# Optimization experiments

Hardware: AMD Instinct MI355X
Metric: run time of the kernel (lower is better)

## Reference

```python
import jax, jax.numpy as jnp
import numpy as np

DIM = 128; MOTION = 128; HEADS = 8; WS = 8; B2 = 4; H = 192; W = 192; HID = 512

def _ln(x, w, b, eps=1e-5):
    m = x.mean(-1, keepdims=True)
    v = ((x - m) ** 2).mean(-1, keepdims=True)
    return (x - m) / jnp.sqrt(v + eps) * w + b

def _win_part(x, ws):
    B, Hh, Ww, C = x.shape
    x = x.reshape(B, Hh // ws, ws, Ww // ws, ws, C).transpose(0, 1, 3, 2, 4, 5)
    return x.reshape(-1, ws * ws, C)

def _win_rev(win, ws, Hh, Ww):
    nwB, N, C = win.shape
    B = nwB // ((Hh // ws) * (Ww // ws))
    x = win.reshape(B, Hh // ws, Ww // ws, ws, ws, C).transpose(0, 1, 3, 2, 4, 5)
    return x.reshape(B, Hh, Ww, C)

def setup_inputs() -> dict:
    key = jax.random.key(0)
    ks = jax.random.split(key, 12)
    def lin(k, o, i):
        return jax.random.normal(k, (o, i), jnp.float32) * 0.02
    return {
        "x": jax.random.normal(ks[0], (B2, H * W, DIM), jnp.float32),
        "cor": jax.random.uniform(ks[1], (B2, H * W, 2), dtype=jnp.float32),
        "q_w": lin(ks[2], DIM, DIM),
        "kv_w": lin(ks[3], 2 * DIM, DIM),
        "cor_w": lin(ks[4], MOTION, 2),
        "proj_w": lin(ks[5], DIM, DIM), "proj_b": jnp.zeros((DIM,), jnp.float32),
        "mproj_w": lin(ks[6], MOTION, MOTION), "mproj_b": jnp.zeros((MOTION,), jnp.float32),
        "norm1_w": jnp.ones((DIM,), jnp.float32), "norm1_b": jnp.zeros((DIM,), jnp.float32),
        "norm2_w": jnp.ones((DIM,), jnp.float32), "norm2_b": jnp.zeros((DIM,), jnp.float32),
        "fc1_w": lin(ks[7], HID, DIM), "fc1_b": jnp.zeros((HID,), jnp.float32),
        "dw_w": jax.random.normal(ks[8], (HID, 1, 3, 3), jnp.float32) * 0.1,
        "dw_b": jnp.zeros((HID,), jnp.float32),
        "fc2_w": lin(ks[9], DIM, HID), "fc2_b": jnp.zeros((DIM,), jnp.float32),
    }

def _attn(x1, x2, cor, q_w, kv_w, cor_w, proj_w, proj_b, mproj_w, mproj_b):
    # x1,x2: (nwB, N, C) windowed query / cross-frame key-value; cor: (nwB, N, 2)
    B, N, C = x1.shape
    hd = C // HEADS
    mh = MOTION // HEADS
    scale = hd ** -0.5
    q = (x1 @ q_w.T).reshape(B, N, HEADS, hd).transpose(0, 2, 1, 3)
    kv = (x2 @ kv_w.T).reshape(B, N, 2, HEADS, hd).transpose(2, 0, 3, 1, 4)
    k, v = kv[0], kv[1]
    ce = cor @ cor_w.T                                   # (B, N, MOTION)
    ceh = ce.reshape(B, N, HEADS, mh).transpose(0, 2, 1, 3)
    attn = jax.nn.softmax(jnp.einsum('bhnd,bhmd->bhnm', q, k) * scale, axis=-1)
    xo = jnp.einsum('bhnm,bhmd->bhnd', attn, v).transpose(0, 2, 1, 3).reshape(B, N, C)
    crev = jnp.einsum('bhnm,bhmd->bhnd', attn, ceh).transpose(0, 2, 1, 3).reshape(B, N, MOTION)
    motion = (crev - ce) @ mproj_w.T + mproj_b
    return xo @ proj_w.T + proj_b, motion

def _mlp(x, fc1_w, fc1_b, dw_w, dw_b, fc2_w, fc2_b):
    B, N, _ = x.shape
    h = x @ fc1_w.T + fc1_b                              # (B, N, HID)
    hm = h.transpose(0, 2, 1).reshape(B, HID, H, W)
    hm = jax.lax.conv_general_dilated(hm, dw_w, (1, 1), 'SAME',
                                      feature_group_count=HID,
                                      dimension_numbers=('NCHW', 'OIHW', 'NCHW'))
    hm = hm + dw_b[None, :, None, None]
    h = jax.nn.gelu(hm.reshape(B, HID, N).transpose(0, 2, 1), approximate=False)
    return h @ fc2_w.T + fc2_b

def reference(x, cor, q_w, kv_w, cor_w, proj_w, proj_b, mproj_w, mproj_b,
              norm1_w, norm1_b, norm2_w, norm2_b, fc1_w, fc1_b, dw_w, dw_b, fc2_w, fc2_b):
    shortcut = x
    xn = _ln(x, norm1_w, norm1_b).reshape(B2, H, W, DIM)
    cm = cor.reshape(B2, H, W, 2)
    xw = _win_part(xn, WS)                               # (nwB, 64, DIM)
    cw = _win_part(cm, WS)
    nwB = xw.shape[0]
    xr = jnp.concatenate([xw[nwB // 2:], xw[:nwB // 2]], axis=0)
    xa, xm = _attn(xw, xr, cw, q_w, kv_w, cor_w, proj_w, proj_b, mproj_w, mproj_b)
    xa = _win_rev(xa, WS, H, W).reshape(B2, H * W, DIM)
    xm = _win_rev(xm, WS, H, W).reshape(B2, H * W, MOTION)
    x = shortcut + xa
    x = x + _mlp(_ln(x, norm2_w, norm2_b), fc1_w, fc1_b, dw_w, dw_b, fc2_w, fc2_b)
    return x, xm
```

## Files before the change

### kernel.cpp

```cpp
#include <hip/hip_runtime.h>
#include <hip/hip_bf16.h>
#include <math.h>

#define NB 4
#define IMG 192
#define HW (IMG*IMG)
#define T_TOT (NB*HW)
#define HID 512
#define NWB 2304
#define WPB 576
#define NWS 24

typedef __bf16 bf16;
typedef __bf16 bf8 __attribute__((ext_vector_type(8)));
typedef __bf16 bf4 __attribute__((ext_vector_type(4)));
typedef float f32x4 __attribute__((ext_vector_type(4)));

#define MFMA(a,b,c) __builtin_amdgcn_mfma_f32_16x16x32_bf16(a,b,c,0,0,0)

__device__ __forceinline__ int swz128(int row, int col){ return row*128 + (col ^ ((row&7)<<3)); }

__device__ __forceinline__ bf8 zero_bf8(){
  bf8 z = { (bf16)0.f,(bf16)0.f,(bf16)0.f,(bf16)0.f,(bf16)0.f,(bf16)0.f,(bf16)0.f,(bf16)0.f };
  return z;
}
__device__ __forceinline__ f32x4 zero_f4(){ f32x4 z = {0.f,0.f,0.f,0.f}; return z; }

__global__ void k_cvt(const float* __restrict__ s, bf16* __restrict__ d, int n, float scale){
  int i = blockIdx.x*256 + threadIdx.x;
  if (i < n) d[i] = (bf16)(s[i]*scale);
}

__global__ void k_a2(const float* __restrict__ mproj_w, const float* __restrict__ cor_w,
                     bf16* __restrict__ a2w){
  int idx = blockIdx.x*256 + threadIdx.x;
  if (idx >= 4096) return;
  int o = idx >> 5, k = idx & 31;
  float acc = 0.f;
  if (k < 16){
    int h = k >> 1, c = k & 1;
    #pragma unroll
    for (int i=0;i<16;i++)
      acc += mproj_w[o*128 + h*16 + i] * cor_w[(h*16+i)*2 + c];
  }
  a2w[o*32 + k] = (bf16)acc;
}

__global__ __launch_bounds__(256) void k_ln1(
    const float* __restrict__ x, const float* __restrict__ cor,
    const float* __restrict__ n1w, const float* __restrict__ n1b,
    bf16* __restrict__ xn, bf16* __restrict__ cwb)
{
  int tid = threadIdx.x, wm = tid>>6, l = tid&63;
  int lr = l & 15, tg = l >> 4;
  int t = blockIdx.x*16 + wm*4 + tg;

  const float* xp = x + (size_t)t*128 + lr*8;
  float4 a = *(const float4*)xp;
  float4 b4 = *(const float4*)(xp+4);
  float s  = a.x+a.y+a.z+a.w + b4.x+b4.y+b4.z+b4.w;
  float sq = a.x*a.x+a.y*a.y+a.z*a.z+a.w*a.w + b4.x*b4.x+b4.y*b4.y+b4.z*b4.z+b4.w*b4.w;
  #pragma unroll
  for (int m=1;m<16;m<<=1){ s += __shfl_xor(s,m,16); sq += __shfl_xor(sq,m,16); }
  float mean = s * (1.0f/128.0f);
  float var  = sq * (1.0f/128.0f) - mean*mean;
  float rstd = rsqrtf(var + 1e-5f);

  float4 nw0 = *(const float4*)(n1w + lr*8), nw1 = *(const float4*)(n1w + lr*8 + 4);
  float4 nb0 = *(const float4*)(n1b + lr*8), nb1 = *(const float4*)(n1b + lr*8 + 4);

  bf8 o;
  o[0] = (bf16)((a.x -mean)*rstd*nw0.x + nb0.x);
  o[1] = (bf16)((a.y -mean)*rstd*nw0.y + nb0.y);
  o[2] = (bf16)((a.z -mean)*rstd*nw0.z + nb0.z);
  o[3] = (bf16)((a.w -mean)*rstd*nw0.w + nb0.w);
  o[4] = (bf16)((b4.x-mean)*rstd*nw1.x + nb1.x);
  o[5] = (bf16)((b4.y-mean)*rstd*nw1.y + nb1.y);
  o[6] = (bf16)((b4.z-mean)*rstd*nw1.z + nb1.z);
  o[7] = (bf16)((b4.w-mean)*rstd*nw1.w + nb1.w);

  int b = t / HW, r = t % HW;
  int yy = r / IMG, xx = r % IMG;
  int win = b*WPB + (yy>>3)*NWS + (xx>>3);
  int n = ((yy&7)<<3) + (xx&7);
  *(bf8*)(xn + (size_t)win*8192 + n*128 + lr*8) = o;

  if (lr < 2) cwb[(size_t)win*128 + n*2 + lr] = (bf16)cor[(size_t)t*2 + lr];
}

__global__ __launch_bounds__(256) void k_attn(
    const bf16* __restrict__ xn, const bf16* __restrict__ cw,
    const bf16* __restrict__ wq, const bf16* __restrict__ wkv,
    const bf16* __restrict__ wpj, const bf16* __restrict__ a2w,
    const float* __restrict__ proj_b, const float* __restrict__ mproj_b,
    const float* __restrict__ x_in, float* __restrict__ x1, float* __restrict__ out_m)
{
  __shared__ __align__(16) bf16 s_s [64*128];
  __shared__ __align__(16) bf16 s_k [64*128];
  __shared__ __align__(16) bf16 s_vT[128*64];
  __shared__ __align__(16) bf16 s_P [2][64*64];
  __shared__ __align__(16) bf16 s_cT[16*64];
  __shared__ __align__(16) bf16 s_D [64*32];

  int tid = threadIdx.x, wm = tid>>6, l = tid&63;
  int lr = l & 15, lg = l >> 4;
  int win = blockIdx.x;
  int partner = (win + NWB/2) % NWB;
  const bf16* xw_g = xn + (size_t)win*8192;
  const bf16* xr_g = xn + (size_t)partner*8192;

  bf8 xrv[4], xwv[4];
  #pragma unroll
  for (int tci=0;tci<4;tci++){
    int chunk = tid + tci*256;
    int row = chunk>>4, c0 = (chunk&15)*8;
    xrv[tci] = *(const bf8*)(xr_g + row*128 + c0);
    xwv[tci] = *(const bf8*)(xw_g + row*128 + c0);
  }
  bf16 cwv = (bf16)0.f;
  if (tid < 128) cwv = cw[(size_t)win*128 + tid];

  *(unsigned long long*)&s_cT[tid*4] = 0ull;
  *(unsigned long long*)&s_D[tid*8]   = 0ull;
  *(unsigned long long*)&s_D[tid*8+4] = 0ull;
  #pragma unroll
  for (int tci=0;tci<4;tci++){
    int chunk = tid + tci*256;
    int row = chunk>>4, c0 = (chunk&15)*8;
    *(bf8*)&s_s[swz128(row,c0)] = xrv[tci];
  }
  __syncthreads();

  if (tid < 128){
    int c = tid & 1, m = tid >> 1;
    s_cT[c*64 + (m ^ (c<<3))] = cwv;
  } else if (tid < 192){
    int m = tid - 128;
    s_cT[2*64 + (m ^ 16)] = (bf16)1.0f;
  }
  {
    bf8 af[4];
    #pragma unroll
    for (int ks=0;ks<4;ks++) af[ks] = *(const bf8*)&s_s[swz128(wm*16+lr, ks*32 + lg*8)];
    #pragma unroll
    for (int nt=0;nt<8;nt++){
      f32x4 acc = zero_f4();
      #pragma unroll
      for (int ks=0;ks<4;ks++){
        bf8 bfr = *(const bf8*)(wkv + (nt*16+lr)*128 + ks*32 + lg*8);
        acc = MFMA(af[ks], bfr, acc);
      }
      #pragma unroll
      for (int j=0;j<4;j++){
        int row = wm*16 + lg*4 + j;
        s_k[swz128(row, nt*16+lr)] = (bf16)acc[j];
      }
    }
    #pragma unroll
    for (int nt=0;nt<8;nt++){
      f32x4 acc = zero_f4();
      #pragma unroll
      for (int ks=0;ks<4;ks++){
        bf8 bfr = *(const bf8*)(wkv + (128 + nt*16+lr)*128 + ks*32 + lg*8);
        acc = MFMA(af[ks], bfr, acc);
      }
      #pragma unroll
      for (int j=0;j<4;j++){
        int tok = wm*16 + lg*4 + j;
        int chc = nt*16 + lr;
        s_vT[chc*64 + (tok ^ ((chc&7)<<3))] = (bf16)acc[j];
      }
    }
  }
  __syncthreads();

  #pragma unroll
  for (int tci=0;tci<4;tci++){
    int chunk = tid + tci*256;
    int row = chunk>>4, c0 = (chunk&15)*8;
    *(bf8*)&s_s[swz128(row,c0)] = xwv[tci];
  }
  __syncthreads();

  {
    bf8 af[4];
    #pragma unroll
    for (int ks=0;ks<4;ks++) af[ks] = *(const bf8*)&s_s[swz128(wm*16+lr, ks*32 + lg*8)];
    #pragma unroll
    for (int nt=0;nt<8;nt++){
      f32x4 acc = zero_f4();
      #pragma unroll
      for (int ks=0;ks<4;ks++){
        bf8 bfr = *(const bf8*)(wq + (nt*16+lr)*128 + ks*32 + lg*8);
        acc = MFMA(af[ks], bfr, acc);
      }
      #pragma unroll
      for (int j=0;j<4;j++){
        int row = wm*16 + lg*4 + j;
        s_s[swz128(row, nt*16+lr)] = (bf16)acc[j];
      }
    }
  }

  float mycw[4] = {0.f,0.f,0.f,0.f};
  if (lr < 2){
    #pragma unroll
    for (int j=0;j<4;j++){
      int row = wm*16 + lg*4 + j;
      mycw[j] = (float)s_cT[lr*64 + (row ^ (lr<<3))];
    }
  }

  #pragma unroll
  for (int h=0;h<8;h++){
    bf8 aS = zero_bf8();
    if (l < 32) aS = *(const bf8*)&s_s[swz128(wm*16+lr, h*16 + lg*8)];
    f32x4 accS[4];
    #pragma unroll
    for (int nt=0;nt<4;nt++){
      bf8 bSv = zero_bf8();
      if (l < 32) bSv = *(const bf8*)&s_k[swz128(nt*16+lr, h*16 + lg*8)];
      accS[nt] = MFMA(aS, bSv, zero_f4());
    }
    bf16* Pb = &s_P[h&1][0];
    #pragma unroll
    for (int nt=0;nt<4;nt++){
      #pragma unroll
      for (int j=0;j<4;j++){
        int row = wm*16 + lg*4 + j;
        Pb[row*64 + ((nt*16+lr) ^ ((row&7)<<3))] = (bf16)__expf(accS[nt][j]);
      }
    }
    f32x4 accO = zero_f4(), accPC = zero_f4();
    #pragma unroll
    for (int ks=0;ks<2;ks++){
      int rowA = wm*16 + lr;
      bf8 aP = *(const bf8*)&Pb[rowA*64 + ((ks*32 + lg*8) ^ ((rowA&7)<<3))];
      int chc = h*16 + lr;
      bf8 bV = *(const bf8*)&s_vT[chc*64 + ((ks*32 + lg*8) ^ ((chc&7)<<3))];
      accO = MFMA(aP, bV, accO);
      bf8 bC = *(const bf8*)&s_cT[lr*64 + ((ks*32 + lg*8) ^ ((lr&7)<<3))];
      accPC = MFMA(aP, bC, accPC);
    }
    #pragma unroll
    for (int j=0;j<4;j++){
      int row = wm*16 + lg*4 + j;
      float rs = __shfl(accPC[j], (l & 48) + 2, 64);
      float inv = __builtin_amdgcn_rcpf(rs);
      s_s[swz128(row, h*16+lr)] = (bf16)(accO[j]*inv);
      if (lr < 2)
        s_D[row*32 + ((2*h+lr) ^ ((row&3)<<3))] = (bf16)(accPC[j]*inv - mycw[j]);
    }
  }

  int b  = win / WPB, wi = win % WPB;
  int wy = wi / NWS,  wx = wi % NWS;
  {
    bf8 af[4];
    #pragma unroll
    for (int ks=0;ks<4;ks++) af[ks] = *(const bf8*)&s_s[swz128(wm*16+lr, ks*32 + lg*8)];
    #pragma unroll
    for (int nt=0;nt<8;nt++){
      f32x4 acc = zero_f4();
      #pragma unroll
      for (int ks=0;ks<4;ks++){
        bf8 bfr = *(const bf8*)(wpj + (nt*16+lr)*128 + ks*32 + lg*8);
        acc = MFMA(af[ks], bfr, acc);
      }
      int col = nt*16 + lr;
      float pb = proj_b[col];
      #pragma unroll
      for (int j=0;j<4;j++){
        int tok = wm*16 + lg*4 + j;
        int yy = wy*8 + (tok>>3), xx = wx*8 + (tok&7);
        size_t addr = ((size_t)b*HW + yy*IMG + xx)*128 + col;
        x1[addr] = acc[j] + pb + x_in[addr];
      }
    }
  }
  {
    int rowA = wm*16 + lr;
    bf8 afD = *(const bf8*)&s_D[rowA*32 + ((lg*8) ^ ((rowA&3)<<3))];
    #pragma unroll
    for (int nt=0;nt<8;nt++){
      bf8 bfr = *(const bf8*)(a2w + (nt*16+lr)*32 + lg*8);
      f32x4 acc = MFMA(afD, bfr, zero_f4());
      int col = nt*16 + lr;
      float pb = mproj_b[col];
      #pragma unroll
      for (int j=0;j<4;j++){
        int tok = wm*16 + lg*4 + j;
        int yy = wy*8 + (tok>>3), xx = wx*8 + (tok&7);
        size_t addr = ((size_t)b*HW + yy*IMG + xx)*128 + col;
        out_m[addr] = acc[j] + pb;
      }
    }
  }
}

__global__ __launch_bounds__(256) void k_fc1(
    const float* __restrict__ x1, const float* __restrict__ n2w, const float* __restrict__ n2b,
    const bf16* __restrict__ wf1, const float* __restrict__ fc1b, bf16* __restrict__ h)
{
  __shared__ __align__(16) bf16 s_a[64*128];
  int tid = threadIdx.x, wm = tid>>6, l = tid&63;
  int lr = l & 15, lg = l >> 4;
  size_t t0 = (size_t)blockIdx.x * 64;

  float4 nw0 = *(const float4*)(n2w + lr*8), nw1 = *(const float4*)(n2w + lr*8 + 4);
  float4 nb0 = *(const float4*)(n2b + lr*8), nb1 = *(const float4*)(n2b + lr*8 + 4);

  #pragma unroll
  for (int rr=0; rr<4; rr++){
    int row = wm*16 + rr*4 + lg;
    const float* xp = x1 + (t0+row)*128 + lr*8;
    float4 a = *(const float4*)xp;
    float4 b4 = *(const float4*)(xp+4);
    float s  = a.x+a.y+a.z+a.w + b4.x+b4.y+b4.z+b4.w;
    float sq = a.x*a.x+a.y*a.y+a.z*a.z+a.w*a.w + b4.x*b4.x+b4.y*b4.y+b4.z*b4.z+b4.w*b4.w;
    #pragma unroll
    for (int m=1;m<16;m<<=1){ s += __shfl_xor(s,m,16); sq += __shfl_xor(sq,m,16); }
    float mean = s*(1.f/128.f), var = sq*(1.f/128.f) - mean*mean;
    float rstd = rsqrtf(var + 1e-5f);
    bf8 o;
    o[0] = (bf16)((a.x -mean)*rstd*nw0.x + nb0.x);
    o[1] = (bf16)((a.y -mean)*rstd*nw0.y + nb0.y);
    o[2] = (bf16)((a.z -mean)*rstd*nw0.z + nb0.z);
    o[3] = (bf16)((a.w -mean)*rstd*nw0.w + nb0.w);
    o[4] = (bf16)((b4.x-mean)*rstd*nw1.x + nb1.x);
    o[5] = (bf16)((b4.y-mean)*rstd*nw1.y + nb1.y);
    o[6] = (bf16)((b4.z-mean)*rstd*nw1.z + nb1.z);
    o[7] = (bf16)((b4.w-mean)*rstd*nw1.w + nb1.w);
    *(bf8*)&s_a[swz128(row, lr*8)] = o;
  }
  __syncthreads();

  bf8 af[4];
  #pragma unroll
  for (int ks=0;ks<4;ks++) af[ks] = *(const bf8*)&s_a[swz128(wm*16+lr, ks*32 + lg*8)];
  for (int ntb=0; ntb<4; ntb++){
    f32x4 acc[8];
    #pragma unroll
    for (int q8=0;q8<8;q8++){
      acc[q8] = zero_f4();
      #pragma unroll
      for (int ks=0;ks<4;ks++){
        int ocol = ntb*128 + q8*16 + lr;
        bf8 bfr = *(const bf8*)(wf1 + (size_t)ocol*128 + ks*32 + lg*8);
        acc[q8] = MFMA(af[ks], bfr, acc[q8]);
      }
    }
    #pragma unroll
    for (int q8=0;q8<8;q8++){
      int col = ntb*128 + q8*16 + lr;
      float bb = fc1b[col];
      #pragma unroll
      for (int j=0;j<4;j++){
        int tl = wm*16 + lg*4 + j;
        h[(t0+tl)*512 + col] = (bf16)(acc[q8][j] + bb);
      }
    }
  }
}

__global__ __launch_bounds__(256) void k_mlp2(
    const bf16* __restrict__ h, const float* __restrict__ dww, const float* __restrict__ dwb,
    const bf16* __restrict__ wf2, const float* __restrict__ fc2b,
    const float* __restrict__ x1, float* __restrict__ outx)
{
  __shared__ __align__(16) bf16 s_hh[100*136];
  int tid = threadIdx.x, wm = tid>>6, l = tid&63;
  int lr = l & 15, lg = l >> 4;
  int tile = 575 - blockIdx.x, b = 3 - blockIdx.y;
  int ty = tile / 24, tx = tile % 24;
  int cq = (tid & 31) * 4;
  int tg2 = tid >> 5;

  f32x4 acc[8];
  #pragma unroll
  for (int q=0;q<8;q++) acc[q] = zero_f4();

  bf8 stg[7];
  #define STAGE_LOAD(KC)                                                     \
    _Pragma("unroll")                                                        \
    for (int it=0; it<7; it++){                                              \
      int idx = it*256 + tid;                                                \
      stg[it] = zero_bf8();                                                  \
      if (idx < 1600){                                                       \
        int pos = idx>>4, c0 = (idx&15)*8;                                   \
        int hy = pos/10, hx = pos%10;                                        \
        int yy = ty*8 + hy - 1, xx = tx*8 + hx - 1;                          \
        if (yy>=0 && yy<IMG && xx>=0 && xx<IMG)                              \
          stg[it] = *(const bf8*)(h + ((size_t)b*HW + yy*IMG + xx)*512 + (KC)*128 + c0); \
      }                                                                      \
    }
  #define STAGE_WRITE()                                                      \
    _Pragma("unroll")                                                        \
    for (int it=0; it<7; it++){                                              \
      int idx = it*256 + tid;                                                \
      if (idx < 1600){                                                       \
        int pos = idx>>4, c0 = (idx&15)*8;                                   \
        *(bf8*)&s_hh[pos*136 + c0] = stg[it];                                \
      }                                                                      \
    }

  STAGE_LOAD(0);
  STAGE_WRITE();
  __syncthreads();

  for (int kc=0;kc<4;kc++){
    if (kc < 3) STAGE_LOAD(kc+1);

    int chg0 = kc*128 + cq;
    float4 bias4 = *(const float4*)(dwb + chg0);
    float cr[8][4];
    #pragma unroll
    for (int i=0;i<8;i++){ cr[i][0]=bias4.x; cr[i][1]=bias4.y; cr[i][2]=bias4.z; cr[i][3]=bias4.w; }
    #pragma unroll
    for (int dy=0;dy<3;dy++){
      #pragma unroll
      for (int dx=0;dx<3;dx++){
        int tq = dy*3+dx;
        float w0 = dww[(chg0+0)*9 + tq];
        float w1 = dww[(chg0+1)*9 + tq];
        float w2 = dww[(chg0+2)*9 + tq];
        float w3 = dww[(chg0+3)*9 + tq];
        #pragma unroll
        for (int i=0;i<8;i++){
          bf4 pv = *(const bf4*)&s_hh[((tg2+dy)*10 + (i+dx))*136 + cq];
          cr[i][0] += (float)pv[0]*w0;
          cr[i][1] += (float)pv[1]*w1;
          cr[i][2] += (float)pv[2]*w2;
          cr[i][3] += (float)pv[3]*w3;
        }
      }
    }
    bf4 gout[8];
    #pragma unroll
    for (int i=0;i<8;i++){
      #pragma unroll
      for (int c=0;c<4;c++){
        float hv = cr[i][c];
        float hv2 = hv*hv;
        float v = hv * fmaf(hv2, -0.0713548353f, -1.5957691216f);
        float g = hv * __builtin_amdgcn_rcpf(1.0f + __expf(v));
        gout[i][c] = (bf16)g;
      }
    }
    __syncthreads();
    #pragma unroll
    for (int i=0;i<8;i++){
      int pos = (tg2+1)*10 + (i+1);
      *(bf4*)&s_hh[pos*136 + (cq ^ (i<<3))] = gout[i];
    }
    {
      bf8 af[4];
      #pragma unroll
      for (int ks=0;ks<4;ks++){
        int tok = wm*16 + lr;
        int pos = ((tok>>3)+1)*10 + (tok&7) + 1;
        af[ks] = *(const bf8*)&s_hh[pos*136 + ((ks*32 + lg*8) ^ ((lr&7)<<3))];
      }
      #pragma unroll
      for (int q=0;q<8;q++){
        #pragma unroll
        for (int ks=0;ks<4;ks++){
          bf8 bfr = *(const bf8*)(wf2 + (size_t)(q*16+lr)*512 + kc*128 + ks*32 + lg*8);
          acc[q] = MFMA(af[ks], bfr, acc[q]);
        }
      }
    }
    if (kc < 3){
      __syncthreads();
      STAGE_WRITE();
      __syncthreads();
    }
  }
  #pragma unroll
  for (int q=0;q<8;q++){
    int col = q*16 + lr;
    float bb = fc2b[col];
    #pragma unroll
    for (int j=0;j<4;j++){
      int tok = wm*16 + lg*4 + j;
      int yy = ty*8 + (tok>>3), xx = tx*8 + (tok&7);
      size_t addr = ((size_t)b*HW + yy*IMG + xx)*128 + col;
      outx[addr] = acc[q][j] + bb + x1[addr];
    }
  }
  #undef STAGE_LOAD
  #undef STAGE_WRITE
}

extern "C" void kernel_launch(void* const* d_in, const int* in_sizes, int n_in,
                              void* d_out, int out_size, void* d_ws, size_t ws_size,
                              hipStream_t stream)
{
  const float* x      = (const float*)d_in[0];
  const float* cor    = (const float*)d_in[1];
  const float* q_w    = (const float*)d_in[2];
  const float* kv_w   = (const float*)d_in[3];
  const float* cor_w  = (const float*)d_in[4];
  const float* proj_w = (const float*)d_in[5];
  const float* proj_b = (const float*)d_in[6];
  const float* mproj_w= (const float*)d_in[7];
  const float* mproj_b= (const float*)d_in[8];
  const float* n1w    = (const float*)d_in[9];
  const float* n1b    = (const float*)d_in[10];
  const float* n2w    = (const float*)d_in[11];
  const float* n2b    = (const float*)d_in[12];
  const float* fc1w   = (const float*)d_in[13];
  const float* fc1b   = (const float*)d_in[14];
  const float* dww    = (const float*)d_in[15];
  const float* dwb    = (const float*)d_in[16];
  const float* fc2w   = (const float*)d_in[17];
  const float* fc2b   = (const float*)d_in[18];
  float* out = (float*)d_out;

  char* ws = (char*)d_ws;
  bf16* wq   = (bf16*)(ws + 0);
  bf16* wkv  = (bf16*)(ws + 32768);
  bf16* wpj  = (bf16*)(ws + 98304);
  bf16* a2w  = (bf16*)(ws + 131072);
  bf16* wf1  = (bf16*)(ws + 139264);
  bf16* wf2  = (bf16*)(ws + 270336);
  bf16* xn   = (bf16*)(ws + 401408);
  bf16* cwb  = (bf16*)(ws + 38150144);
  float* x1  = (float*)(ws + 38739968);
  bf16* hbuf = (bf16*)(ws + 114237440);

  k_cvt<<<64,  256, 0, stream>>>(q_w,   wq,  16384, 0.25f);
  k_cvt<<<128, 256, 0, stream>>>(kv_w,  wkv, 32768, 1.0f);
  k_cvt<<<64,  256, 0, stream>>>(proj_w,wpj, 16384, 1.0f);
  k_cvt<<<256, 256, 0, stream>>>(fc1w,  wf1, 65536, 1.0f);
  k_cvt<<<256, 256, 0, stream>>>(fc2w,  wf2, 65536, 1.0f);
  k_a2 <<<16,  256, 0, stream>>>(mproj_w, cor_w, a2w);

  k_ln1 <<<T_TOT/16, 256, 0, stream>>>(x, cor, n1w, n1b, xn, cwb);
  k_attn<<<NWB,      256, 0, stream>>>(xn, cwb, wq, wkv, wpj, a2w, proj_b, mproj_b,
                                       x, x1, out + (size_t)T_TOT*128);
  k_fc1 <<<T_TOT/64, 256, 0, stream>>>(x1, n2w, n2b, wf1, fc1b, hbuf);
  k_mlp2<<<dim3(576,4), 256, 0, stream>>>(hbuf, dww, dwb, wf2, fc2b, x1, out);
}
```

Baseline: 544.0 us.

## Fuse LayerNorm2 and fc1 into attention kernel epilogue; reuse dwconv rows in registers

Removes the separate fc1 kernel. The attention kernel now keeps the post-residual x1 values in registers, runs LayerNorm2 across the 16-lane groups, writes the normalized rows to shared memory, and computes fc1 directly into the hidden buffer at spatial token addresses. This avoids re-reading x1 from global memory and saves a kernel launch, but raises register pressure and makes the attention kernel longer. Separately, the depthwise conv loads each row of 10 pixels from LDS once per dy and reuses them across the dx taps, cutting redundant shared-memory reads.

```diff
diff --git a/kernel.cpp b/kernel.cpp
--- a/kernel.cpp
+++ b/kernel.cpp
@@ -93,7 +93,10 @@
     const bf16* __restrict__ wq, const bf16* __restrict__ wkv,
     const bf16* __restrict__ wpj, const bf16* __restrict__ a2w,
     const float* __restrict__ proj_b, const float* __restrict__ mproj_b,
-    const float* __restrict__ x_in, float* __restrict__ x1, float* __restrict__ out_m)
+    const float* __restrict__ x_in, float* __restrict__ x1, float* __restrict__ out_m,
+    const float* __restrict__ n2w, const float* __restrict__ n2b,
+    const bf16* __restrict__ wf1, const float* __restrict__ fc1b,
+    bf16* __restrict__ hb)
 {
   __shared__ __align__(16) bf16 s_s [64*128];
   __shared__ __align__(16) bf16 s_k [64*128];
@@ -255,6 +258,15 @@
 
   int b  = win / WPB, wi = win % WPB;
   int wy = wi / NWS,  wx = wi % NWS;
+  size_t ta[4];
+  #pragma unroll
+  for (int j=0;j<4;j++){
+    int tok = wm*16 + lg*4 + j;
+    int yy = wy*8 + (tok>>3), xx2 = wx*8 + (tok&7);
+    ta[j] = (size_t)b*HW + yy*IMG + xx2;
+  }
+
+  float xv[8][4];
   {
     bf8 af[4];
     #pragma unroll
@@ -271,10 +283,51 @@
       float pb = proj_b[col];
       #pragma unroll
       for (int j=0;j<4;j++){
-        int tok = wm*16 + lg*4 + j;
-        int yy = wy*8 + (tok>>3), xx = wx*8 + (tok&7);
-        size_t addr = ((size_t)b*HW + yy*IMG + xx)*128 + col;
-        x1[addr] = acc[j] + pb + x_in[addr];
+        size_t addr = ta[j]*128 + col;
+        float v = acc[j] + pb + x_in[addr];
+        x1[addr] = v;
+        xv[nt][j] = v;
+      }
+    }
+  }
+  {
+    float w2r[8], b2r[8];
+    #pragma unroll
+    for (int nt=0;nt<8;nt++){ w2r[nt] = n2w[nt*16+lr]; b2r[nt] = n2b[nt*16+lr]; }
+    #pragma unroll
+    for (int j=0;j<4;j++){
+      float s=0.f, sq=0.f;
+      #pragma unroll
+      for (int nt=0;nt<8;nt++){ float v = xv[nt][j]; s += v; sq += v*v; }
+      #pragma unroll
+      for (int m=1;m<16;m<<=1){ s += __shfl_xor(s,m,16); sq += __shfl_xor(sq,m,16); }
+      float mean = s*(1.f/128.f), var = sq*(1.f/128.f) - mean*mean;
+      float rstd = rsqrtf(var + 1e-5f);
+      int row = wm*16 + lg*4 + j;
+      #pragma unroll
+      for (int nt=0;nt<8;nt++)
+        s_s[swz128(row, nt*16+lr)] = (bf16)((xv[nt][j]-mean)*rstd*w2r[nt] + b2r[nt]);
+    }
+  }
+  {
+    bf8 af[4];
+    #pragma unroll
+    for (int ks=0;ks<4;ks++) af[ks] = *(const bf8*)&s_s[swz128(wm*16+lr, ks*32 + lg*8)];
+    for (int ntb=0; ntb<4; ntb++){
+      #pragma unroll
+      for (int q8=0;q8<8;q8++){
+        f32x4 acc = zero_f4();
+        #pragma unroll
+        for (int ks=0;ks<4;ks++){
+          int ocol = ntb*128 + q8*16 + lr;
+          bf8 bfr = *(const bf8*)(wf1 + (size_t)ocol*128 + ks*32 + lg*8);
+          acc = MFMA(af[ks], bfr, acc);
+        }
+        int col = ntb*128 + q8*16 + lr;
+        float bb = fc1b[col];
+        #pragma unroll
+        for (int j=0;j<4;j++)
+          hb[ta[j]*512 + col] = (bf16)(acc[j] + bb);
       }
     }
   }
@@ -288,77 +341,8 @@
       int col = nt*16 + lr;
       float pb = mproj_b[col];
       #pragma unroll
-      for (int j=0;j<4;j++){
-        int tok = wm*16 + lg*4 + j;
-        int yy = wy*8 + (tok>>3), xx = wx*8 + (tok&7);
-        size_t addr = ((size_t)b*HW + yy*IMG + xx)*128 + col;
-        out_m[addr] = acc[j] + pb;
-      }
-    }
-  }
-}
-
-__global__ __launch_bounds__(256) void k_fc1(
-    const float* __restrict__ x1, const float* __restrict__ n2w, const float* __restrict__ n2b,
-    const bf16* __restrict__ wf1, const float* __restrict__ fc1b, bf16* __restrict__ h)
-{
-  __shared__ __align__(16) bf16 s_a[64*128];
-  int tid = threadIdx.x, wm = tid>>6, l = tid&63;
-  int lr = l & 15, lg = l >> 4;
-  size_t t0 = (size_t)blockIdx.x * 64;
-
-  float4 nw0 = *(const float4*)(n2w + lr*8), nw1 = *(const float4*)(n2w + lr*8 + 4);
-  float4 nb0 = *(const float4*)(n2b + lr*8), nb1 = *(const float4*)(n2b + lr*8 + 4);
-
-  #pragma unroll
-  for (int rr=0; rr<4; rr++){
-    int row = wm*16 + rr*4 + lg;
-    const float* xp = x1 + (t0+row)*128 + lr*8;
-    float4 a = *(const float4*)xp;
-    float4 b4 = *(const float4*)(xp+4);
-    float s  = a.x+a.y+a.z+a.w + b4.x+b4.y+b4.z+b4.w;
-    float sq = a.x*a.x+a.y*a.y+a.z*a.z+a.w*a.w + b4.x*b4.x+b4.y*b4.y+b4.z*b4.z+b4.w*b4.w;
-    #pragma unroll
-    for (int m=1;m<16;m<<=1){ s += __shfl_xor(s,m,16); sq += __shfl_xor(sq,m,16); }
-    float mean = s*(1.f/128.f), var = sq*(1.f/128.f) - mean*mean;
-    float rstd = rsqrtf(var + 1e-5f);
-    bf8 o;
-    o[0] = (bf16)((a.x -mean)*rstd*nw0.x + nb0.x);
-    o[1] = (bf16)((a.y -mean)*rstd*nw0.y + nb0.y);
-    o[2] = (bf16)((a.z -mean)*rstd*nw0.z + nb0.z);
-    o[3] = (bf16)((a.w -mean)*rstd*nw0.w + nb0.w);
-    o[4] = (bf16)((b4.x-mean)*rstd*nw1.x + nb1.x);
-    o[5] = (bf16)((b4.y-mean)*rstd*nw1.y + nb1.y);
-    o[6] = (bf16)((b4.z-mean)*rstd*nw1.z + nb1.z);
-    o[7] = (bf16)((b4.w-mean)*rstd*nw1.w + nb1.w);
-    *(bf8*)&s_a[swz128(row, lr*8)] = o;
-  }
-  __syncthreads();
-
-  bf8 af[4];
-  #pragma unroll
-  for (int ks=0;ks<4;ks++) af[ks] = *(const bf8*)&s_a[swz128(wm*16+lr, ks*32 + lg*8)];
-  for (int ntb=0; ntb<4; ntb++){
-    f32x4 acc[8];
-    #pragma unroll
-    for (int q8=0;q8<8;q8++){
-      acc[q8] = zero_f4();
-      #pragma unroll
-      for (int ks=0;ks<4;ks++){
-        int ocol = ntb*128 + q8*16 + lr;
-        bf8 bfr = *(const bf8*)(wf1 + (size_t)ocol*128 + ks*32 + lg*8);
-        acc[q8] = MFMA(af[ks], bfr, acc[q8]);
-      }
-    }
-    #pragma unroll
-    for (int q8=0;q8<8;q8++){
-      int col = ntb*128 + q8*16 + lr;
-      float bb = fc1b[col];
-      #pragma unroll
-      for (int j=0;j<4;j++){
-        int tl = wm*16 + lg*4 + j;
-        h[(t0+tl)*512 + col] = (bf16)(acc[q8][j] + bb);
-      }
+      for (int j=0;j<4;j++)
+        out_m[ta[j]*128 + col] = acc[j] + pb;
     }
   }
 }
@@ -418,6 +402,13 @@
     for (int i=0;i<8;i++){ cr[i][0]=bias4.x; cr[i][1]=bias4.y; cr[i][2]=bias4.z; cr[i][3]=bias4.w; }
     #pragma unroll
     for (int dy=0;dy<3;dy++){
+      float rv[10][4];
+      #pragma unroll
+      for (int p=0;p<10;p++){
+        bf4 pv = *(const bf4*)&s_hh[((tg2+dy)*10 + p)*136 + cq];
+        rv[p][0]=(float)pv[0]; rv[p][1]=(float)pv[1];
+        rv[p][2]=(float)pv[2]; rv[p][3]=(float)pv[3];
+      }
       #pragma unroll
       for (int dx=0;dx<3;dx++){
         int tq = dy*3+dx;
@@ -427,11 +418,10 @@
         float w3 = dww[(chg0+3)*9 + tq];
         #pragma unroll
         for (int i=0;i<8;i++){
-          bf4 pv = *(const bf4*)&s_hh[((tg2+dy)*10 + (i+dx))*136 + cq];
-          cr[i][0] += (float)pv[0]*w0;
-          cr[i][1] += (float)pv[1]*w1;
-          cr[i][2] += (float)pv[2]*w2;
-          cr[i][3] += (float)pv[3]*w3;
+          cr[i][0] += rv[i+dx][0]*w0;
+          cr[i][1] += rv[i+dx][1]*w1;
+          cr[i][2] += rv[i+dx][2]*w2;
+          cr[i][3] += rv[i+dx][3]*w3;
         }
       }
     }
@@ -538,7 +528,7 @@
 
   k_ln1 <<<T_TOT/16, 256, 0, stream>>>(x, cor, n1w, n1b, xn, cwb);
   k_attn<<<NWB,      256, 0, stream>>>(xn, cwb, wq, wkv, wpj, a2w, proj_b, mproj_b,
-                                       x, x1, out + (size_t)T_TOT*128);
-  k_fc1 <<<T_TOT/64, 256, 0, stream>>>(x1, n2w, n2b, wf1, fc1b, hbuf);
+                                       x, x1, out + (size_t)T_TOT*128,
+                                       n2w, n2b, wf1, fc1b, hbuf);
   k_mlp2<<<dim3(576,4), 256, 0, stream>>>(hbuf, dww, dwb, wf2, fc2b, x1, out);
 }
```

After: 629.5 us. 1.16x slower.
